# Kernel optimization log

Measured on AMD Instinct MI355X. Metric: run time of the kernel, lower is better.

Reference implementation:

```python
import jax, jax.numpy as jnp
import numpy as np

TEXTURE_W, SHAPE_W, INTENSITY_W = 1.0, 0.5, 1.0
EPS = 1e-08


def _conv2d_same(x, k):
    # x: [B,1,H,W], k: [1,1,3,3], zero padding 1 (SAME)
    return jax.lax.conv_general_dilated(
        x, k, window_strides=(1, 1), padding='SAME',
        dimension_numbers=('NCHW', 'OIHW', 'NCHW'))


def _box_mean(x):
    # mean over 3x3 zero-padded window == F.unfold(k=3,pad=1).mean(dim=1) for C=1
    k = jnp.ones((1, 1, 3, 3), x.dtype) / 9.0
    return _conv2d_same(x, k)


def _local_variance(x):
    # mean((patch - patch_mean)^2) == E[x^2] - E[x]^2 over the padded 3x3 window
    m = _box_mean(x)
    m2 = _box_mean(x * x)
    return m2 - m * m


def _intensity_loss(inp, out, mask):
    ms = mask.sum() + EPS
    im = (inp * mask).sum() / ms
    om = (out * mask).sum() / ms
    di, do = inp - im, out - om
    iv = (di * di * mask).sum() / ms
    ov = (do * do * mask).sum() / ms
    isk = (di ** 3 * mask).sum() / (ms * (iv ** 1.5 + EPS))
    osk = (do ** 3 * mask).sum() / (ms * (ov ** 1.5 + EPS))
    iku = (di ** 4 * mask).sum() / (ms * (iv ** 2 + EPS))
    oku = (do ** 4 * mask).sum() / (ms * (ov ** 2 + EPS))
    return (im - om) ** 2 + (iv - ov) ** 2 + (isk - osk) ** 2 + (iku - oku) ** 2


def _texture_loss(inp, out, mask):
    it = _local_variance(inp)
    ot = _local_variance(out)
    return jnp.abs(ot * mask - it * mask).mean()


def _shape_loss(inp, out, mask):
    lap = jnp.array([[0., 1., 0.], [1., -4., 1.], [0., 1., 0.]], inp.dtype).reshape(1, 1, 3, 3)
    il = _conv2d_same(inp, lap)
    ol = _conv2d_same(out, lap)
    return jnp.abs(ol * mask - il * mask).mean()


def setup_inputs() -> dict:
    key = jax.random.key(0)
    k1, k2, k3 = jax.random.split(key, 3)
    shape = (32, 1, 512, 512)
    return {
        'input_img': jax.random.normal(k1, shape, jnp.float32),
        'output_img': jax.random.normal(k2, shape, jnp.float32),
        'roi_mask': jax.random.uniform(k3, shape, jnp.float32),
    }


def reference(input_img, output_img, roi_mask):
    intensity = _intensity_loss(input_img, output_img, roi_mask)
    texture = _texture_loss(input_img, output_img, roi_mask)
    shape = _shape_loss(input_img, output_img, roi_mask)
    total = INTENSITY_W * intensity + TEXTURE_W * texture + SHAPE_W * shape
    # stacked [intensity, texture, shape, total] (dict values in original order)
    return jnp.stack([intensity, texture, shape, total])
```

## Files before the change

kernel.cpp:

```cpp
#include <hip/hip_runtime.h>
#include <math.h>

#define H 512
#define W 512
#define BAND 4
#define NQ 11

__device__ __forceinline__ float shfl_up1(float v, int lane) {
    float r = __shfl_up(v, 1);
    return (lane == 0) ? 0.0f : r;
}
__device__ __forceinline__ float shfl_dn1(float v, int lane) {
    float r = __shfl_down(v, 1);
    return (lane == 63) ? 0.0f : r;
}

__device__ __forceinline__ void load_row(const float* __restrict__ base, size_t img_off,
                                         int y, int x0, float* dst) {
    if (y < 0 || y >= H) {
        #pragma unroll
        for (int j = 0; j < 8; j++) dst[j] = 0.0f;
    } else {
        const float4* p = reinterpret_cast<const float4*>(base + img_off + (size_t)y * W + x0);
        float4 a = p[0];
        float4 b = p[1];
        dst[0] = a.x; dst[1] = a.y; dst[2] = a.z; dst[3] = a.w;
        dst[4] = b.x; dst[5] = b.y; dst[6] = b.z; dst[7] = b.w;
    }
}

__global__ __launch_bounds__(256) void radiomics_main(
    const float* __restrict__ inp, const float* __restrict__ outp,
    const float* __restrict__ mask, double* __restrict__ partials)
{
    const int tid = threadIdx.x;
    const int lane = tid & 63;
    const int wib = tid >> 6;
    const int gwave = blockIdx.x * 4 + wib;
    const int b = gwave >> 7;
    const int band = gwave & 127;
    const int y0 = band * BAND;
    const size_t off = (size_t)b * H * W;
    const int x0 = lane * 8;

    float Pi[8], Ci[8], Ni[8];
    float Po[8], Co[8], No[8];
    float Mk[8];

    load_row(inp,  off, y0 - 1, x0, Pi);
    load_row(inp,  off, y0,     x0, Ci);
    load_row(inp,  off, y0 + 1, x0, Ni);
    load_row(outp, off, y0 - 1, x0, Po);
    load_row(outp, off, y0,     x0, Co);
    load_row(outp, off, y0 + 1, x0, No);
    load_row(mask, off, y0,     x0, Mk);

    float acc[NQ];
    #pragma unroll
    for (int q = 0; q < NQ; q++) acc[q] = 0.0f;

    const float inv9 = 1.0f / 9.0f;

    #pragma unroll
    for (int i = 0; i < BAND; i++) {
        if (i) {
            #pragma unroll
            for (int j = 0; j < 8; j++) { Pi[j] = Ci[j]; Ci[j] = Ni[j]; Po[j] = Co[j]; Co[j] = No[j]; }
            load_row(inp,  off, y0 + i + 1, x0, Ni);
            load_row(outp, off, y0 + i + 1, x0, No);
            load_row(mask, off, y0 + i,     x0, Mk);
        }

        float t1[8], t2[8];
        float tvm[8], lpm[8];

        #pragma unroll
        for (int j = 0; j < 8; j++) {
            t1[j] = Pi[j] + Ci[j] + Ni[j];
            t2[j] = fmaf(Pi[j], Pi[j], fmaf(Ci[j], Ci[j], Ni[j] * Ni[j]));
        }
        {
            float h1l = shfl_up1(t1[7], lane), h1r = shfl_dn1(t1[0], lane);
            float h2l = shfl_up1(t2[7], lane), h2r = shfl_dn1(t2[0], lane);
            float hcl = shfl_up1(Ci[7], lane), hcr = shfl_dn1(Ci[0], lane);
            #pragma unroll
            for (int j = 0; j < 8; j++) {
                float l1 = (j == 0) ? h1l : t1[j-1];
                float r1 = (j == 7) ? h1r : t1[j+1];
                float l2 = (j == 0) ? h2l : t2[j-1];
                float r2 = (j == 7) ? h2r : t2[j+1];
                float mn = (l1 + t1[j] + r1) * inv9;
                float tv = fmaf(-mn, mn, (l2 + t2[j] + r2) * inv9);
                float cl = (j == 0) ? hcl : Ci[j-1];
                float cr = (j == 7) ? hcr : Ci[j+1];
                float lp = (t1[j] - Ci[j]) + cl + cr - 4.0f * Ci[j];
                tvm[j] = tv * Mk[j];
                lpm[j] = lp * Mk[j];
            }
        }

        #pragma unroll
        for (int j = 0; j < 8; j++) {
            t1[j] = Po[j] + Co[j] + No[j];
            t2[j] = fmaf(Po[j], Po[j], fmaf(Co[j], Co[j], No[j] * No[j]));
        }
        {
            float h1l = shfl_up1(t1[7], lane), h1r = shfl_dn1(t1[0], lane);
            float h2l = shfl_up1(t2[7], lane), h2r = shfl_dn1(t2[0], lane);
            float hcl = shfl_up1(Co[7], lane), hcr = shfl_dn1(Co[0], lane);
            #pragma unroll
            for (int j = 0; j < 8; j++) {
                float l1 = (j == 0) ? h1l : t1[j-1];
                float r1 = (j == 7) ? h1r : t1[j+1];
                float l2 = (j == 0) ? h2l : t2[j-1];
                float r2 = (j == 7) ? h2r : t2[j+1];
                float mn = (l1 + t1[j] + r1) * inv9;
                float tv = fmaf(-mn, mn, (l2 + t2[j] + r2) * inv9);
                float cl = (j == 0) ? hcl : Co[j-1];
                float cr = (j == 7) ? hcr : Co[j+1];
                float lp = (t1[j] - Co[j]) + cl + cr - 4.0f * Co[j];
                acc[9]  += fabsf(tv * Mk[j] - tvm[j]);
                acc[10] += fabsf(lp * Mk[j] - lpm[j]);
            }
        }

        #pragma unroll
        for (int j = 0; j < 8; j++) {
            float m = Mk[j];
            acc[0] += m;
            float xi = Ci[j];
            float t = xi * m; acc[1] += t; t *= xi; acc[2] += t; t *= xi; acc[3] += t; t *= xi; acc[4] += t;
            float xo = Co[j];
            t = xo * m; acc[5] += t; t *= xo; acc[6] += t; t *= xo; acc[7] += t; t *= xo; acc[8] += t;
        }
    }

    #pragma unroll
    for (int q = 0; q < NQ; q++) {
        float v = acc[q];
        #pragma unroll
        for (int o = 32; o > 0; o >>= 1) v += __shfl_down(v, o);
        acc[q] = v;
    }
    __shared__ double red[4][NQ];
    if (lane == 0) {
        #pragma unroll
        for (int q = 0; q < NQ; q++) red[wib][q] = (double)acc[q];
    }
    __syncthreads();
    if (tid < NQ) {
        double s = red[0][tid] + red[1][tid] + red[2][tid] + red[3][tid];
        partials[(size_t)blockIdx.x * NQ + tid] = s;
    }
}

__global__ __launch_bounds__(256) void radiomics_final(
    const double* __restrict__ partials, int nblk, float* __restrict__ out4, double inv_n)
{
    const int tid = threadIdx.x;
    const int lane = tid & 63;
    const int w = tid >> 6;
    double q[NQ];
    #pragma unroll
    for (int k = 0; k < NQ; k++) q[k] = 0.0;
    for (int i = tid; i < nblk; i += 256) {
        #pragma unroll
        for (int k = 0; k < NQ; k++) q[k] += partials[(size_t)i * NQ + k];
    }
    #pragma unroll
    for (int k = 0; k < NQ; k++) {
        #pragma unroll
        for (int o = 32; o > 0; o >>= 1) q[k] += __shfl_down(q[k], o);
    }
    __shared__ double red[4][NQ];
    if (lane == 0) {
        #pragma unroll
        for (int k = 0; k < NQ; k++) red[w][k] = q[k];
    }
    __syncthreads();
    if (tid == 0) {
        double s[NQ];
        #pragma unroll
        for (int k = 0; k < NQ; k++) s[k] = red[0][k] + red[1][k] + red[2][k] + red[3][k];
        const double EPS = 1e-8;
        double S0 = s[0];
        double ms = S0 + EPS;
        double im = s[1] / ms, om = s[5] / ms;
        double im2 = im * im, im3 = im2 * im, im4 = im2 * im2;
        double om2 = om * om, om3 = om2 * om, om4 = om2 * om2;
        double di2 = s[2] - 2.0*im*s[1] + im2*S0;
        double do2 = s[6] - 2.0*om*s[5] + om2*S0;
        double iv = di2 / ms, ov = do2 / ms;
        double di3 = s[3] - 3.0*im*s[2] + 3.0*im2*s[1] - im3*S0;
        double do3 = s[7] - 3.0*om*s[6] + 3.0*om2*s[5] - om3*S0;
        double isk = di3 / (ms * (iv * sqrt(iv) + EPS));
        double osk = do3 / (ms * (ov * sqrt(ov) + EPS));
        double di4 = s[4] - 4.0*im*s[3] + 6.0*im2*s[2] - 4.0*im3*s[1] + im4*S0;
        double do4 = s[8] - 4.0*om*s[7] + 6.0*om2*s[6] - 4.0*om3*s[5] + om4*S0;
        double iku = di4 / (ms * (iv * iv + EPS));
        double oku = do4 / (ms * (ov * ov + EPS));
        double intensity = (im-om)*(im-om) + (iv-ov)*(iv-ov)
                         + (isk-osk)*(isk-osk) + (iku-oku)*(iku-oku);
        double texture = s[9]  * inv_n;
        double shape   = s[10] * inv_n;
        double total = intensity + texture + 0.5 * shape;
        out4[0] = (float)intensity;
        out4[1] = (float)texture;
        out4[2] = (float)shape;
        out4[3] = (float)total;
    }
}

extern "C" void kernel_launch(void* const* d_in, const int* in_sizes, int n_in,
                              void* d_out, int out_size, void* d_ws, size_t ws_size,
                              hipStream_t stream) {
    const float* inp  = (const float*)d_in[0];
    const float* outp = (const float*)d_in[1];
    const float* mask = (const float*)d_in[2];
    const int total = in_sizes[0];
    const int nimg  = total / (H * W);
    const int nwaves = nimg * (H / BAND);
    const int nblk   = nwaves / 4;
    double* partials = (double*)d_ws;

    radiomics_main<<<nblk, 256, 0, stream>>>(inp, outp, mask, partials);
    const double inv_n = 1.0 / (double)total;
    radiomics_final<<<1, 256, 0, stream>>>(partials, nblk, (float*)d_out, inv_n);
}
```

Measured before the change: 127.2 us.

## Stage image bands in LDS via async global-to-LDS copies

Each block now processes an 8-row band of one image. It copies the 10 input and output rows it needs (band plus halo) into LDS with asynchronous global_load_lds, and each wave then computes two rows by reading 10-wide neighbourhoods from LDS. The old design had every wave load 6 rows for 4 output rows and fetch horizontal neighbours with lane shuffles. The change is meant to cut redundant halo traffic and shuffles and to give more memory-level parallelism. In exchange it uses about 40KB of LDS per block, which can limit occupancy, and it relies on the async LDS copies being complete at the barrier.

```diff
diff --git a/kernel.cpp b/kernel.cpp
--- a/kernel.cpp
+++ b/kernel.cpp
@@ -3,135 +3,129 @@
 
 #define H 512
 #define W 512
-#define BAND 4
+#define BAND 8
+#define STAGE (BAND + 2)
 #define NQ 11
 
-__device__ __forceinline__ float shfl_up1(float v, int lane) {
-    float r = __shfl_up(v, 1);
-    return (lane == 0) ? 0.0f : r;
-}
-__device__ __forceinline__ float shfl_dn1(float v, int lane) {
-    float r = __shfl_down(v, 1);
-    return (lane == 63) ? 0.0f : r;
-}
-
-__device__ __forceinline__ void load_row(const float* __restrict__ base, size_t img_off,
-                                         int y, int x0, float* dst) {
-    if (y < 0 || y >= H) {
-        #pragma unroll
-        for (int j = 0; j < 8; j++) dst[j] = 0.0f;
-    } else {
-        const float4* p = reinterpret_cast<const float4*>(base + img_off + (size_t)y * W + x0);
-        float4 a = p[0];
-        float4 b = p[1];
-        dst[0] = a.x; dst[1] = a.y; dst[2] = a.z; dst[3] = a.w;
-        dst[4] = b.x; dst[5] = b.y; dst[6] = b.z; dst[7] = b.w;
-    }
+typedef __attribute__((address_space(3))) void       lds_void;
+typedef const __attribute__((address_space(1))) void g_void;
+
+__device__ __forceinline__ void async_copy16(const float* g, float* l) {
+    __builtin_amdgcn_global_load_lds((g_void*)g, (lds_void*)l, 16, 0, 0);
+}
+
+__device__ __forceinline__ void load10(const float* row, int x0, float* a) {
+    float4 u = *(const float4*)&row[x0];
+    float4 v = *(const float4*)&row[x0 + 4];
+    a[0] = (x0 == 0) ? 0.0f : row[x0 - 1];
+    a[1] = u.x; a[2] = u.y; a[3] = u.z; a[4] = u.w;
+    a[5] = v.x; a[6] = v.y; a[7] = v.z; a[8] = v.w;
+    a[9] = (x0 + 8 == W) ? 0.0f : row[x0 + 8];
 }
 
 __global__ __launch_bounds__(256) void radiomics_main(
     const float* __restrict__ inp, const float* __restrict__ outp,
     const float* __restrict__ mask, double* __restrict__ partials)
 {
-    const int tid = threadIdx.x;
+    __shared__ float lds[2][STAGE][W];
+
+    const int tid  = threadIdx.x;
     const int lane = tid & 63;
-    const int wib = tid >> 6;
-    const int gwave = blockIdx.x * 4 + wib;
-    const int b = gwave >> 7;
-    const int band = gwave & 127;
-    const int y0 = band * BAND;
+    const int wib  = tid >> 6;
+    const int blk  = blockIdx.x;
+    const int b    = blk >> 6;
+    const int band = blk & 63;
+    const int y0   = band * BAND;
     const size_t off = (size_t)b * H * W;
-    const int x0 = lane * 8;
-
-    float Pi[8], Ci[8], Ni[8];
-    float Po[8], Co[8], No[8];
-    float Mk[8];
-
-    load_row(inp,  off, y0 - 1, x0, Pi);
-    load_row(inp,  off, y0,     x0, Ci);
-    load_row(inp,  off, y0 + 1, x0, Ni);
-    load_row(outp, off, y0 - 1, x0, Po);
-    load_row(outp, off, y0,     x0, Co);
-    load_row(outp, off, y0 + 1, x0, No);
-    load_row(mask, off, y0,     x0, Mk);
-
+    const int x0   = lane * 8;
+
+    for (int s = wib; s < 2 * STAGE * 2; s += 4) {
+        const int img = s / (2 * STAGE);
+        const int rem = s - img * (2 * STAGE);
+        const int rs  = rem >> 1;
+        const int g   = rem & 1;
+        const int y   = y0 - 1 + rs;
+        float* dst = &lds[img][rs][g * 256];
+        if (y < 0 || y >= H) {
+            *(float4*)&dst[lane * 4] = make_float4(0.f, 0.f, 0.f, 0.f);
+        } else {
+            const float* src = (img ? outp : inp) + off + (size_t)y * W + g * 256 + lane * 4;
+            async_copy16(src, dst);
+        }
+    }
+
+    const int r0 = y0 + 2 * wib;
+    float Mk[16];
+    {
+        const float4* p = (const float4*)(mask + off + (size_t)r0 * W + x0);
+        float4 a = p[0], c = p[1];
+        const float4* q = (const float4*)(mask + off + (size_t)(r0 + 1) * W + x0);
+        float4 d = q[0], e = q[1];
+        Mk[0]=a.x; Mk[1]=a.y; Mk[2]=a.z; Mk[3]=a.w; Mk[4]=c.x; Mk[5]=c.y; Mk[6]=c.z; Mk[7]=c.w;
+        Mk[8]=d.x; Mk[9]=d.y; Mk[10]=d.z; Mk[11]=d.w; Mk[12]=e.x; Mk[13]=e.y; Mk[14]=e.z; Mk[15]=e.w;
+    }
+
+    __syncthreads();
+
+    const float inv9 = 1.0f / 9.0f;
     float acc[NQ];
     #pragma unroll
     for (int q = 0; q < NQ; q++) acc[q] = 0.0f;
 
-    const float inv9 = 1.0f / 9.0f;
-
-    #pragma unroll
-    for (int i = 0; i < BAND; i++) {
-        if (i) {
-            #pragma unroll
-            for (int j = 0; j < 8; j++) { Pi[j] = Ci[j]; Ci[j] = Ni[j]; Po[j] = Co[j]; Co[j] = No[j]; }
-            load_row(inp,  off, y0 + i + 1, x0, Ni);
-            load_row(outp, off, y0 + i + 1, x0, No);
-            load_row(mask, off, y0 + i,     x0, Mk);
-        }
-
-        float t1[8], t2[8];
-        float tvm[8], lpm[8];
-
-        #pragma unroll
-        for (int j = 0; j < 8; j++) {
-            t1[j] = Pi[j] + Ci[j] + Ni[j];
-            t2[j] = fmaf(Pi[j], Pi[j], fmaf(Ci[j], Ci[j], Ni[j] * Ni[j]));
+    #pragma unroll
+    for (int cr = 0; cr < 2; cr++) {
+        const int rs = 2 * wib + cr + 1;
+        const float* mrow = &Mk[cr * 8];
+        float tvI[8], lpI[8];
+
+        {
+            float A[10], B[10], C[10];
+            load10(lds[0][rs - 1], x0, A);
+            load10(lds[0][rs],     x0, B);
+            load10(lds[0][rs + 1], x0, C);
+            float c1[10], c2[10];
+            #pragma unroll
+            for (int j = 0; j < 10; j++) {
+                c1[j] = A[j] + B[j] + C[j];
+                c2[j] = fmaf(A[j], A[j], fmaf(B[j], B[j], C[j] * C[j]));
+            }
+            #pragma unroll
+            for (int j = 0; j < 8; j++) {
+                float s1 = c1[j] + c1[j+1] + c1[j+2];
+                float s2 = c2[j] + c2[j+1] + c2[j+2];
+                float mn = s1 * inv9;
+                tvI[j] = fmaf(-mn, mn, s2 * inv9);
+                lpI[j] = A[j+1] + C[j+1] + B[j] + B[j+2] - 4.0f * B[j+1];
+                float m = mrow[j];
+                acc[0] += m;
+                float x = B[j+1];
+                float t = x * m; acc[1] += t; t *= x; acc[2] += t; t *= x; acc[3] += t; t *= x; acc[4] += t;
+            }
         }
         {
-            float h1l = shfl_up1(t1[7], lane), h1r = shfl_dn1(t1[0], lane);
-            float h2l = shfl_up1(t2[7], lane), h2r = shfl_dn1(t2[0], lane);
-            float hcl = shfl_up1(Ci[7], lane), hcr = shfl_dn1(Ci[0], lane);
+            float A[10], B[10], C[10];
+            load10(lds[1][rs - 1], x0, A);
+            load10(lds[1][rs],     x0, B);
+            load10(lds[1][rs + 1], x0, C);
+            float c1[10], c2[10];
+            #pragma unroll
+            for (int j = 0; j < 10; j++) {
+                c1[j] = A[j] + B[j] + C[j];
+                c2[j] = fmaf(A[j], A[j], fmaf(B[j], B[j], C[j] * C[j]));
+            }
             #pragma unroll
             for (int j = 0; j < 8; j++) {
-                float l1 = (j == 0) ? h1l : t1[j-1];
-                float r1 = (j == 7) ? h1r : t1[j+1];
-                float l2 = (j == 0) ? h2l : t2[j-1];
-                float r2 = (j == 7) ? h2r : t2[j+1];
-                float mn = (l1 + t1[j] + r1) * inv9;
-                float tv = fmaf(-mn, mn, (l2 + t2[j] + r2) * inv9);
-                float cl = (j == 0) ? hcl : Ci[j-1];
-                float cr = (j == 7) ? hcr : Ci[j+1];
-                float lp = (t1[j] - Ci[j]) + cl + cr - 4.0f * Ci[j];
-                tvm[j] = tv * Mk[j];
-                lpm[j] = lp * Mk[j];
-            }
-        }
-
-        #pragma unroll
-        for (int j = 0; j < 8; j++) {
-            t1[j] = Po[j] + Co[j] + No[j];
-            t2[j] = fmaf(Po[j], Po[j], fmaf(Co[j], Co[j], No[j] * No[j]));
-        }
-        {
-            float h1l = shfl_up1(t1[7], lane), h1r = shfl_dn1(t1[0], lane);
-            float h2l = shfl_up1(t2[7], lane), h2r = shfl_dn1(t2[0], lane);
-            float hcl = shfl_up1(Co[7], lane), hcr = shfl_dn1(Co[0], lane);
-            #pragma unroll
-            for (int j = 0; j < 8; j++) {
-                float l1 = (j == 0) ? h1l : t1[j-1];
-                float r1 = (j == 7) ? h1r : t1[j+1];
-                float l2 = (j == 0) ? h2l : t2[j-1];
-                float r2 = (j == 7) ? h2r : t2[j+1];
-                float mn = (l1 + t1[j] + r1) * inv9;
-                float tv = fmaf(-mn, mn, (l2 + t2[j] + r2) * inv9);
-                float cl = (j == 0) ? hcl : Co[j-1];
-                float cr = (j == 7) ? hcr : Co[j+1];
-                float lp = (t1[j] - Co[j]) + cl + cr - 4.0f * Co[j];
-                acc[9]  += fabsf(tv * Mk[j] - tvm[j]);
-                acc[10] += fabsf(lp * Mk[j] - lpm[j]);
-            }
-        }
-
-        #pragma unroll
-        for (int j = 0; j < 8; j++) {
-            float m = Mk[j];
-            acc[0] += m;
-            float xi = Ci[j];
-            float t = xi * m; acc[1] += t; t *= xi; acc[2] += t; t *= xi; acc[3] += t; t *= xi; acc[4] += t;
-            float xo = Co[j];
-            t = xo * m; acc[5] += t; t *= xo; acc[6] += t; t *= xo; acc[7] += t; t *= xo; acc[8] += t;
+                float s1 = c1[j] + c1[j+1] + c1[j+2];
+                float s2 = c2[j] + c2[j+1] + c2[j+2];
+                float mn = s1 * inv9;
+                float tv = fmaf(-mn, mn, s2 * inv9);
+                float lp = A[j+1] + C[j+1] + B[j] + B[j+2] - 4.0f * B[j+1];
+                float m = mrow[j];
+                acc[9]  += fabsf(tv * m - tvI[j] * m);
+                acc[10] += fabsf(lp * m - lpI[j] * m);
+                float x = B[j+1];
+                float t = x * m; acc[5] += t; t *= x; acc[6] += t; t *= x; acc[7] += t; t *= x; acc[8] += t;
+            }
         }
     }
 
@@ -142,15 +136,17 @@
         for (int o = 32; o > 0; o >>= 1) v += __shfl_down(v, o);
         acc[q] = v;
     }
-    __shared__ double red[4][NQ];
+    __syncthreads();
+    float* rf = (float*)lds;
     if (lane == 0) {
         #pragma unroll
-        for (int q = 0; q < NQ; q++) red[wib][q] = (double)acc[q];
+        for (int q = 0; q < NQ; q++) rf[wib * NQ + q] = acc[q];
     }
     __syncthreads();
     if (tid < NQ) {
-        double s = red[0][tid] + red[1][tid] + red[2][tid] + red[3][tid];
-        partials[(size_t)blockIdx.x * NQ + tid] = s;
+        double s = (double)rf[tid] + (double)rf[NQ + tid]
+                 + (double)rf[2 * NQ + tid] + (double)rf[3 * NQ + tid];
+        partials[(size_t)blk * NQ + tid] = s;
     }
 }
 
@@ -219,8 +215,7 @@
     const float* mask = (const float*)d_in[2];
     const int total = in_sizes[0];
     const int nimg  = total / (H * W);
-    const int nwaves = nimg * (H / BAND);
-    const int nblk   = nwaves / 4;
+    const int nblk  = nimg * (H / BAND);
     double* partials = (double*)d_ws;
 
     radiomics_main<<<nblk, 256, 0, stream>>>(inp, outp, mask, partials);
```

Measured after the change: 131.1 us. 3.1% more time.
